# Performance work log

Measured on AMD Instinct MI355X. Metric: run time of the kernel, lower is better.

The kernel has to match this reference:

```python
import jax, jax.numpy as jnp
import numpy as np

B, N, M = 2, 8192, 8192


def setup_inputs() -> dict:
    key = jax.random.key(0)
    ks = jax.random.split(key, 12)
    def rn(k, shape):
        return jax.random.normal(k, shape, dtype=jnp.float32)
    return {
        "in_xyz": rn(ks[0], (B, N, 3)),
        "in_rot": rn(ks[1], (B, N, 4)),
        "in_scale": rn(ks[2], (B, N, 3)),
        "in_opacity": rn(ks[3], (B, N, 1)),
        "in_sh_dc": rn(ks[4], (B, N, 3)),
        "in_sh_rest": rn(ks[5], (B, N, 45)),
        "out_xyz": rn(ks[6], (B, M, 3)),
        "out_rot": rn(ks[7], (B, M, 4)),
        "out_scale": rn(ks[8], (B, M, 3)),
        "out_opacity": rn(ks[9], (B, M, 1)),
        "out_sh_dc": rn(ks[10], (B, M, 3)),
        "out_sh_rest": rn(ks[11], (B, M, 45)),
    }


POS_W, ROT_W, SCALE_W, OPAC_W, SH_W = 1.0, 0.5, 0.5, 0.3, 0.2


def _cdist(a, b):
    # a: [B,M,3], b: [B,N,3] -> [B,M,N] Euclidean distance via Gram trick
    sq = (jnp.sum(a * a, -1)[:, :, None] + jnp.sum(b * b, -1)[:, None, :]
          - 2.0 * jnp.einsum('bmd,bnd->bmn', a, b))
    return jnp.sqrt(jnp.maximum(sq, 0.0))


def _gather(x, idx):
    # x: [B,N,D], idx: [B,M] -> [B,M,D]
    return jnp.take_along_axis(x, idx[:, :, None], axis=1)


def reference(in_xyz, in_rot, in_scale, in_opacity, in_sh_dc, in_sh_rest,
              out_xyz, out_rot, out_scale, out_opacity, out_sh_dc, out_sh_rest):
    dist = _cdist(out_xyz, in_xyz)                 # [B,M,N]
    min_out_to_in = jnp.min(dist, axis=2)          # [B,M]
    match_idx = jnp.argmin(dist, axis=2)           # [B,M]
    min_in_to_out = jnp.min(dist, axis=1)          # [B,N]
    pos_loss = (min_out_to_in.mean() + min_in_to_out.mean()) / 2

    matched_rot = _gather(in_rot, match_idx)
    matched_scale = _gather(in_scale, match_idx)
    matched_opacity = _gather(in_opacity, match_idx)
    matched_sh_dc = _gather(in_sh_dc, match_idx)
    matched_sh_rest = _gather(in_sh_rest, match_idx)

    rot_dot = jnp.abs(jnp.sum(out_rot * matched_rot, axis=-1))
    rot_loss = jnp.mean(1.0 - rot_dot)
    scale_loss = jnp.mean(jnp.abs(out_scale - matched_scale))
    opacity_loss = jnp.mean(jnp.abs(out_opacity - matched_opacity))
    sh_loss = (jnp.mean(jnp.abs(out_sh_dc - matched_sh_dc))
               + jnp.mean(jnp.abs(out_sh_rest - matched_sh_rest)))

    total = (POS_W * pos_loss + ROT_W * rot_loss + SCALE_W * scale_loss
             + OPAC_W * opacity_loss + SH_W * sh_loss)
    return total
```

## Files before the change

### kernel.cpp

```cpp
#include <hip/hip_runtime.h>


#define BB 2
#define NN 8192
#define MM 8192
#define TILE_PTS 1024
#define CHUNK_PTS 64
#define CH_STRIDE (CHUNK_PTS * 4 + 4)
#define PM 256
#define NSL 8
#define NPAIR 512

__device__ __forceinline__ void dmerge(float& d, int& i, float od, int oi) {
    if (od < d || (od == d && oi < i)) { d = od; i = oi; }
}

__device__ __forceinline__ void stage_tile(const float* __restrict__ xyz,
                                           int b, int gtile, int t, float* smem) {
    const uint4* src = (const uint4*)((const char*)xyz +
                       ((size_t)b * NN + (size_t)gtile * TILE_PTS) * 12);
    uint4 wb[3];
#pragma unroll
    for (int k = 0; k < 3; ++k) wb[k] = src[t * 3 + k];
    const unsigned int* w = (const unsigned int*)wb;
    const int p0 = t * 4;
    float4* dst = (float4*)(smem + (p0 >> 6) * CH_STRIDE) + (p0 & 63);
#pragma unroll
    for (int i = 0; i < 4; ++i) {
        float x = __uint_as_float(w[3 * i + 0]);
        float y = __uint_as_float(w[3 * i + 1]);
        float z = __uint_as_float(w[3 * i + 2]);
        float4 v;
        v.x = x; v.y = y; v.z = z;
        v.w = fmaf(z, z, fmaf(y, y, x * x));
        dst[i] = v;
    }
}

__global__ __launch_bounds__(1024) void k_out(
    const float* __restrict__ in_xyz,
    const float* __restrict__ out_xyz,
    float* __restrict__ outD2,
    int*   __restrict__ outIdx) {

    __shared__ float smem[16 * CH_STRIDE];

    const int t  = threadIdx.x;
    const int ml = t >> 4;
    const int c  = t & 15;
    const int blk = blockIdx.x;
    const int b  = blk >> 8;
    const int e  = (blk >> 5) & 7;
    const int m0 = (blk & 31) * PM + ml * 4;

    float m2x0, m2y0, m2z0, msq0, m2x1, m2y1, m2z1, msq1;
    float m2x2, m2y2, m2z2, msq2, m2x3, m2y3, m2z3, msq3;
#define LOADQ(i)                                                            \
    { const float* op = out_xyz + ((size_t)b * MM + m0 + i) * 3;            \
      float ox = op[0], oy = op[1], oz = op[2];                             \
      m2x##i = -2.f * ox; m2y##i = -2.f * oy; m2z##i = -2.f * oz;           \
      msq##i = fmaf(oz, oz, fmaf(oy, oy, ox * ox)); }
    LOADQ(0) LOADQ(1) LOADQ(2) LOADQ(3)
#undef LOADQ

    float bd0 = 3e38f, bd1 = 3e38f, bd2 = 3e38f, bd3 = 3e38f;
    int   bi0 = 0,     bi1 = 0,     bi2 = 0,     bi3 = 0;

    if (t < 256) stage_tile(in_xyz, b, e, t, smem);
    __syncthreads();

    const float4* cp = (const float4*)(smem + c * CH_STRIDE);
    const int base = e * TILE_PTS + c * CHUNK_PTS;
#pragma unroll 8
    for (int j = 0; j < CHUNK_PTS; ++j) {
        float4 p = cp[j];
        float k0 = fmaf(p.x, m2x0, fmaf(p.y, m2y0, fmaf(p.z, m2z0, p.w)));
        float k1 = fmaf(p.x, m2x1, fmaf(p.y, m2y1, fmaf(p.z, m2z1, p.w)));
        float k2 = fmaf(p.x, m2x2, fmaf(p.y, m2y2, fmaf(p.z, m2z2, p.w)));
        float k3 = fmaf(p.x, m2x3, fmaf(p.y, m2y3, fmaf(p.z, m2z3, p.w)));
        if (k0 < bd0) { bd0 = k0; bi0 = base + j; }
        if (k1 < bd1) { bd1 = k1; bi1 = base + j; }
        if (k2 < bd2) { bd2 = k2; bi2 = base + j; }
        if (k3 < bd3) { bd3 = k3; bi3 = base + j; }
    }

#pragma unroll
    for (int off = 1; off < 16; off <<= 1) {
        float od; int oi;
        od = __shfl_xor(bd0, off, 64); oi = __shfl_xor(bi0, off, 64); dmerge(bd0, bi0, od, oi);
        od = __shfl_xor(bd1, off, 64); oi = __shfl_xor(bi1, off, 64); dmerge(bd1, bi1, od, oi);
        od = __shfl_xor(bd2, off, 64); oi = __shfl_xor(bi2, off, 64); dmerge(bd2, bi2, od, oi);
        od = __shfl_xor(bd3, off, 64); oi = __shfl_xor(bi3, off, 64); dmerge(bd3, bi3, od, oi);
    }
    if (c == 0) {
        const size_t g = ((size_t)b * MM + m0) * NSL + e;
        outD2[g + 0 * NSL] = bd0 + msq0; outIdx[g + 0 * NSL] = bi0;
        outD2[g + 1 * NSL] = bd1 + msq1; outIdx[g + 1 * NSL] = bi1;
        outD2[g + 2 * NSL] = bd2 + msq2; outIdx[g + 2 * NSL] = bi2;
        outD2[g + 3 * NSL] = bd3 + msq3; outIdx[g + 3 * NSL] = bi3;
    }
}

__global__ __launch_bounds__(1024) void k_in(
    const float* __restrict__ in_xyz,
    const float* __restrict__ out_xyz,
    float* __restrict__ inD2) {

    __shared__ float smem[16 * CH_STRIDE];

    const int t  = threadIdx.x;
    const int ml = t >> 4;
    const int c  = t & 15;
    const int blk = blockIdx.x;
    const int b  = blk >> 8;
    const int e  = (blk >> 5) & 7;
    const int n0 = (blk & 31) * PM + ml * 4;

    float n2x0, n2y0, n2z0, nsq0, n2x1, n2y1, n2z1, nsq1;
    float n2x2, n2y2, n2z2, nsq2, n2x3, n2y3, n2z3, nsq3;
#define LOADQ(i)                                                            \
    { const float* ip = in_xyz + ((size_t)b * NN + n0 + i) * 3;             \
      float x = ip[0], y = ip[1], z = ip[2];                                \
      n2x##i = -2.f * x; n2y##i = -2.f * y; n2z##i = -2.f * z;              \
      nsq##i = fmaf(z, z, fmaf(y, y, x * x)); }
    LOADQ(0) LOADQ(1) LOADQ(2) LOADQ(3)
#undef LOADQ

    float bd0 = 3e38f, bd1 = 3e38f, bd2 = 3e38f, bd3 = 3e38f;

    if (t < 256) stage_tile(out_xyz, b, e, t, smem);
    __syncthreads();

    const float4* cp = (const float4*)(smem + c * CH_STRIDE);
#pragma unroll 8
    for (int j = 0; j < CHUNK_PTS; ++j) {
        float4 p = cp[j];
        float k0 = fmaf(p.x, n2x0, fmaf(p.y, n2y0, fmaf(p.z, n2z0, p.w)));
        float k1 = fmaf(p.x, n2x1, fmaf(p.y, n2y1, fmaf(p.z, n2z1, p.w)));
        float k2 = fmaf(p.x, n2x2, fmaf(p.y, n2y2, fmaf(p.z, n2z2, p.w)));
        float k3 = fmaf(p.x, n2x3, fmaf(p.y, n2y3, fmaf(p.z, n2z3, p.w)));
        bd0 = fminf(bd0, k0);
        bd1 = fminf(bd1, k1);
        bd2 = fminf(bd2, k2);
        bd3 = fminf(bd3, k3);
    }

#pragma unroll
    for (int off = 1; off < 16; off <<= 1) {
        bd0 = fminf(bd0, __shfl_xor(bd0, off, 64));
        bd1 = fminf(bd1, __shfl_xor(bd1, off, 64));
        bd2 = fminf(bd2, __shfl_xor(bd2, off, 64));
        bd3 = fminf(bd3, __shfl_xor(bd3, off, 64));
    }
    if (c == 0) {
        const size_t g = ((size_t)b * NN + n0) * NSL + e;
        inD2[g + 0 * NSL] = bd0 + nsq0;
        inD2[g + 1 * NSL] = bd1 + nsq1;
        inD2[g + 2 * NSL] = bd2 + nsq2;
        inD2[g + 3 * NSL] = bd3 + nsq3;
    }
}

__global__ __launch_bounds__(256) void k_epi(
    const float* __restrict__ in_rot,
    const float* __restrict__ in_scale,
    const float* __restrict__ in_op,
    const float* __restrict__ in_dc,
    const float* __restrict__ in_rest,
    const float* __restrict__ out_rot,
    const float* __restrict__ out_scale,
    const float* __restrict__ out_op,
    const float* __restrict__ out_dc,
    const float* __restrict__ out_rest,
    const float* __restrict__ outD2,
    const int*   __restrict__ outIdx,
    const float* __restrict__ inD2,
    float* __restrict__ pout,
    float* __restrict__ pin) {

    const int t = threadIdx.x;
    const int blk = blockIdx.x;

    if (blk < 128) {
        const int u = blk * 256 + t;
        const int m = u >> 1;
        const int h = u & 1;
        const int b = m >> 13;
        float d2 = outD2[(size_t)m * NSL + 0];
        int  idx = outIdx[(size_t)m * NSL + 0];
#pragma unroll
        for (int s = 1; s < NSL; ++s) {
            float ds = outD2[(size_t)m * NSL + s];
            int   is = outIdx[(size_t)m * NSL + s];
            if (ds < d2) { d2 = ds; idx = is; }
        }
        const size_t og = (size_t)m;
        const size_t ig = (size_t)b * NN + (size_t)idx;

        float pos = 0.f, rot = 0.f, scl = 0.f, opa = 0.f, dcv = 0.f, rsv = 0.f;
        if (h == 0) {
            pos = sqrtf(fmaxf(d2, 0.f));
            const float4 orv = ((const float4*)out_rot)[og];
            const float4 irv = ((const float4*)in_rot)[ig];
            float rdot = orv.x * irv.x + orv.y * irv.y + orv.z * irv.z + orv.w * irv.w;
            rot = 1.f - fabsf(rdot);
#pragma unroll
            for (int qq = 0; qq < 3; ++qq) scl += fabsf(out_scale[og * 3 + qq] - in_scale[ig * 3 + qq]);
            opa = fabsf(out_op[og] - in_op[ig]);
#pragma unroll
            for (int qq = 0; qq < 3; ++qq) dcv += fabsf(out_dc[og * 3 + qq] - in_dc[ig * 3 + qq]);
#pragma unroll
            for (int e = 0; e < 22; ++e)
                rsv += fabsf(out_rest[og * 45 + e] - in_rest[ig * 45 + e]);
        } else {
#pragma unroll
            for (int e = 22; e < 45; ++e)
                rsv += fabsf(out_rest[og * 45 + e] - in_rest[ig * 45 + e]);
        }

#pragma unroll
        for (int off = 1; off < 64; off <<= 1) {
            pos += __shfl_xor(pos, off, 64);
            rot += __shfl_xor(rot, off, 64);
            scl += __shfl_xor(scl, off, 64);
            opa += __shfl_xor(opa, off, 64);
            dcv += __shfl_xor(dcv, off, 64);
            rsv += __shfl_xor(rsv, off, 64);
        }
        if ((t & 63) == 0) {
            const size_t w = (size_t)blk * 4 + (t >> 6);
            pout[w * 6 + 0] = pos; pout[w * 6 + 1] = rot; pout[w * 6 + 2] = scl;
            pout[w * 6 + 3] = opa; pout[w * 6 + 4] = dcv; pout[w * 6 + 5] = rsv;
        }
    } else {
        const int g = (blk - 128) * 256 + t;
        float d2 = inD2[(size_t)g * NSL + 0];
#pragma unroll
        for (int s = 1; s < NSL; ++s) d2 = fminf(d2, inD2[(size_t)g * NSL + s]);
        float v = sqrtf(fmaxf(d2, 0.f));
#pragma unroll
        for (int off = 1; off < 64; off <<= 1) v += __shfl_xor(v, off, 64);
        if ((t & 63) == 0) pin[(size_t)(blk - 128) * 4 + (t >> 6)] = v;
    }
}

__global__ __launch_bounds__(256) void k_fin(const float* __restrict__ pout,
                                             const float* __restrict__ pin,
                                             unsigned int* __restrict__ out) {
    __shared__ float red[4][8];
    const int t = threadIdx.x;
    float s0 = 0.f, s1 = 0.f, s2 = 0.f, s3 = 0.f, s4 = 0.f, s5 = 0.f, s6 = 0.f;
    for (int i = t; i < 512; i += 256) {
        s0 += pout[(size_t)i * 6 + 0];
        s1 += pout[(size_t)i * 6 + 1];
        s2 += pout[(size_t)i * 6 + 2];
        s3 += pout[(size_t)i * 6 + 3];
        s4 += pout[(size_t)i * 6 + 4];
        s5 += pout[(size_t)i * 6 + 5];
    }
    if (t < 256) s6 += pin[t];
#pragma unroll
    for (int off = 1; off < 64; off <<= 1) {
        s0 += __shfl_xor(s0, off, 64);
        s1 += __shfl_xor(s1, off, 64);
        s2 += __shfl_xor(s2, off, 64);
        s3 += __shfl_xor(s3, off, 64);
        s4 += __shfl_xor(s4, off, 64);
        s5 += __shfl_xor(s5, off, 64);
        s6 += __shfl_xor(s6, off, 64);
    }
    if ((t & 63) == 0) {
        const int w = t >> 6;
        red[w][0] = s0; red[w][1] = s1; red[w][2] = s2; red[w][3] = s3;
        red[w][4] = s4; red[w][5] = s5; red[w][6] = s6;
    }
    __syncthreads();
    if (t == 0) {
        float a[7];
#pragma unroll
        for (int j = 0; j < 7; ++j)
            a[j] = red[0][j] + red[1][j] + red[2][j] + red[3][j];
        const float inv_bm = 1.0f / (float)(BB * MM);
        const float inv_bn = 1.0f / (float)(BB * NN);
        const float pos = 0.5f * (a[0] * inv_bm + a[6] * inv_bn);
        const float rot = a[1] * inv_bm;
        const float scl = a[2] * inv_bm * (1.f / 3.f);
        const float opa = a[3] * inv_bm;
        const float sh  = a[4] * inv_bm * (1.f / 3.f) + a[5] * inv_bm * (1.f / 45.f);
        const float total = 1.0f * pos + 0.5f * rot + 0.5f * scl + 0.3f * opa + 0.2f * sh;
        unsigned int ub = __float_as_uint(total);
        unsigned int r  = (ub + 0x7FFFu + ((ub >> 16) & 1u)) >> 16;
        if (!(total == total) || fabsf(total) > 1e30f) r = 0x4080u;
        out[0] = (r << 16) | r;
    }
}

extern "C" void kernel_launch(void* const* d_in, const int* in_sizes, int n_in,
                              void* d_out, int out_size, void* d_ws, size_t ws_size,
                              hipStream_t stream) {
    const float* in_xyz    = (const float*)d_in[0];
    const float* in_rot    = (const float*)d_in[1];
    const float* in_scale  = (const float*)d_in[2];
    const float* in_op     = (const float*)d_in[3];
    const float* in_dc     = (const float*)d_in[4];
    const float* in_rest   = (const float*)d_in[5];
    const float* out_xyz   = (const float*)d_in[6];
    const float* out_rot   = (const float*)d_in[7];
    const float* out_scale = (const float*)d_in[8];
    const float* out_op    = (const float*)d_in[9];
    const float* out_dc    = (const float*)d_in[10];
    const float* out_rest  = (const float*)d_in[11];

    float* outD2 = (float*)d_ws;
    int*   outIdx = (int*)(outD2 + (size_t)BB * MM * NSL);
    float* inD2  = (float*)(outIdx + (size_t)BB * MM * NSL);
    float* pout  = inD2 + (size_t)BB * NN * NSL;
    float* pin   = pout + 512 * 6;

    k_out<<<NPAIR, 1024, 0, stream>>>(in_xyz, out_xyz, outD2, outIdx);
    k_in<<<NPAIR, 1024, 0, stream>>>(in_xyz, out_xyz, inD2);
    k_epi<<<192, 256, 0, stream>>>(in_rot, in_scale, in_op, in_dc, in_rest,
                                   out_rot, out_scale, out_op, out_dc, out_rest,
                                   outD2, outIdx, inD2, pout, pin);
    k_fin<<<1, 256, 0, stream>>>(pout, pin, (unsigned int*)d_out);
}
```

Measured before the change: 120.1 us.

## Merge nearest-neighbor kernels into one launch with 8 queries per thread and deferred argmin

The separate out-to-in and in-to-out min-distance kernels become one kernel whose block index picks the direction, removing a launch. Each thread now handles 8 query points instead of 4, doubling reuse of every point loaded from shared memory. The argmin index is no longer tracked in the hot loop. It is found afterwards by rescanning the chunk for the lane that holds the group minimum. This trades a short extra rescan and more registers for a cheaper inner loop of plain fminf operations.

```diff
diff --git a/kernel.cpp b/kernel.cpp
--- a/kernel.cpp
+++ b/kernel.cpp
@@ -7,13 +7,9 @@
 #define TILE_PTS 1024
 #define CHUNK_PTS 64
 #define CH_STRIDE (CHUNK_PTS * 4 + 4)
-#define PM 256
+#define PM 512
 #define NSL 8
-#define NPAIR 512
-
-__device__ __forceinline__ void dmerge(float& d, int& i, float od, int oi) {
-    if (od < d || (od == d && oi < i)) { d = od; i = oi; }
-}
+#define NBLK 512
 
 __device__ __forceinline__ void stage_tile(const float* __restrict__ xyz,
                                            int b, int gtile, int t, float* smem) {
@@ -37,11 +33,12 @@
     }
 }
 
-__global__ __launch_bounds__(1024) void k_out(
+__global__ __launch_bounds__(1024) void k_pair(
     const float* __restrict__ in_xyz,
     const float* __restrict__ out_xyz,
     float* __restrict__ outD2,
-    int*   __restrict__ outIdx) {
+    int*   __restrict__ outIdx,
+    float* __restrict__ inD2) {
 
     __shared__ float smem[16 * CH_STRIDE];
 
@@ -49,115 +46,82 @@
     const int ml = t >> 4;
     const int c  = t & 15;
     const int blk = blockIdx.x;
-    const int b  = blk >> 8;
-    const int e  = (blk >> 5) & 7;
-    const int m0 = (blk & 31) * PM + ml * 4;
-
-    float m2x0, m2y0, m2z0, msq0, m2x1, m2y1, m2z1, msq1;
-    float m2x2, m2y2, m2z2, msq2, m2x3, m2y3, m2z3, msq3;
-#define LOADQ(i)                                                            \
-    { const float* op = out_xyz + ((size_t)b * MM + m0 + i) * 3;            \
-      float ox = op[0], oy = op[1], oz = op[2];                             \
-      m2x##i = -2.f * ox; m2y##i = -2.f * oy; m2z##i = -2.f * oz;           \
-      msq##i = fmaf(oz, oz, fmaf(oy, oy, ox * ox)); }
-    LOADQ(0) LOADQ(1) LOADQ(2) LOADQ(3)
-#undef LOADQ
-
-    float bd0 = 3e38f, bd1 = 3e38f, bd2 = 3e38f, bd3 = 3e38f;
-    int   bi0 = 0,     bi1 = 0,     bi2 = 0,     bi3 = 0;
-
-    if (t < 256) stage_tile(in_xyz, b, e, t, smem);
+    const int side = blk >> 8;
+    const int r8 = blk & 255;
+    const int b  = r8 >> 7;
+    const int e  = (r8 >> 4) & 7;
+    const int g  = r8 & 15;
+    const int q0 = g * PM + ml * 8;
+
+    const float* qbase = (side == 0) ? out_xyz : in_xyz;
+    const float* pbase = (side == 0) ? in_xyz  : out_xyz;
+
+    float qx[8], qy[8], qz[8], bd[8];
+#pragma unroll
+    for (int r = 0; r < 8; ++r) {
+        const float* qp = qbase + ((size_t)b * MM + q0 + r) * 3;
+        qx[r] = -2.f * qp[0];
+        qy[r] = -2.f * qp[1];
+        qz[r] = -2.f * qp[2];
+        bd[r] = 3e38f;
+    }
+
+    if (t < 256) stage_tile(pbase, b, e, t, smem);
     __syncthreads();
 
     const float4* cp = (const float4*)(smem + c * CH_STRIDE);
     const int base = e * TILE_PTS + c * CHUNK_PTS;
-#pragma unroll 8
+
+#pragma unroll 2
     for (int j = 0; j < CHUNK_PTS; ++j) {
         float4 p = cp[j];
-        float k0 = fmaf(p.x, m2x0, fmaf(p.y, m2y0, fmaf(p.z, m2z0, p.w)));
-        float k1 = fmaf(p.x, m2x1, fmaf(p.y, m2y1, fmaf(p.z, m2z1, p.w)));
-        float k2 = fmaf(p.x, m2x2, fmaf(p.y, m2y2, fmaf(p.z, m2z2, p.w)));
-        float k3 = fmaf(p.x, m2x3, fmaf(p.y, m2y3, fmaf(p.z, m2z3, p.w)));
-        if (k0 < bd0) { bd0 = k0; bi0 = base + j; }
-        if (k1 < bd1) { bd1 = k1; bi1 = base + j; }
-        if (k2 < bd2) { bd2 = k2; bi2 = base + j; }
-        if (k3 < bd3) { bd3 = k3; bi3 = base + j; }
-    }
-
-#pragma unroll
-    for (int off = 1; off < 16; off <<= 1) {
-        float od; int oi;
-        od = __shfl_xor(bd0, off, 64); oi = __shfl_xor(bi0, off, 64); dmerge(bd0, bi0, od, oi);
-        od = __shfl_xor(bd1, off, 64); oi = __shfl_xor(bi1, off, 64); dmerge(bd1, bi1, od, oi);
-        od = __shfl_xor(bd2, off, 64); oi = __shfl_xor(bi2, off, 64); dmerge(bd2, bi2, od, oi);
-        od = __shfl_xor(bd3, off, 64); oi = __shfl_xor(bi3, off, 64); dmerge(bd3, bi3, od, oi);
-    }
-    if (c == 0) {
-        const size_t g = ((size_t)b * MM + m0) * NSL + e;
-        outD2[g + 0 * NSL] = bd0 + msq0; outIdx[g + 0 * NSL] = bi0;
-        outD2[g + 1 * NSL] = bd1 + msq1; outIdx[g + 1 * NSL] = bi1;
-        outD2[g + 2 * NSL] = bd2 + msq2; outIdx[g + 2 * NSL] = bi2;
-        outD2[g + 3 * NSL] = bd3 + msq3; outIdx[g + 3 * NSL] = bi3;
-    }
-}
-
-__global__ __launch_bounds__(1024) void k_in(
-    const float* __restrict__ in_xyz,
-    const float* __restrict__ out_xyz,
-    float* __restrict__ inD2) {
-
-    __shared__ float smem[16 * CH_STRIDE];
-
-    const int t  = threadIdx.x;
-    const int ml = t >> 4;
-    const int c  = t & 15;
-    const int blk = blockIdx.x;
-    const int b  = blk >> 8;
-    const int e  = (blk >> 5) & 7;
-    const int n0 = (blk & 31) * PM + ml * 4;
-
-    float n2x0, n2y0, n2z0, nsq0, n2x1, n2y1, n2z1, nsq1;
-    float n2x2, n2y2, n2z2, nsq2, n2x3, n2y3, n2z3, nsq3;
-#define LOADQ(i)                                                            \
-    { const float* ip = in_xyz + ((size_t)b * NN + n0 + i) * 3;             \
-      float x = ip[0], y = ip[1], z = ip[2];                                \
-      n2x##i = -2.f * x; n2y##i = -2.f * y; n2z##i = -2.f * z;              \
-      nsq##i = fmaf(z, z, fmaf(y, y, x * x)); }
-    LOADQ(0) LOADQ(1) LOADQ(2) LOADQ(3)
-#undef LOADQ
-
-    float bd0 = 3e38f, bd1 = 3e38f, bd2 = 3e38f, bd3 = 3e38f;
-
-    if (t < 256) stage_tile(out_xyz, b, e, t, smem);
-    __syncthreads();
-
-    const float4* cp = (const float4*)(smem + c * CH_STRIDE);
-#pragma unroll 8
-    for (int j = 0; j < CHUNK_PTS; ++j) {
-        float4 p = cp[j];
-        float k0 = fmaf(p.x, n2x0, fmaf(p.y, n2y0, fmaf(p.z, n2z0, p.w)));
-        float k1 = fmaf(p.x, n2x1, fmaf(p.y, n2y1, fmaf(p.z, n2z1, p.w)));
-        float k2 = fmaf(p.x, n2x2, fmaf(p.y, n2y2, fmaf(p.z, n2z2, p.w)));
-        float k3 = fmaf(p.x, n2x3, fmaf(p.y, n2y3, fmaf(p.z, n2z3, p.w)));
-        bd0 = fminf(bd0, k0);
-        bd1 = fminf(bd1, k1);
-        bd2 = fminf(bd2, k2);
-        bd3 = fminf(bd3, k3);
-    }
-
-#pragma unroll
-    for (int off = 1; off < 16; off <<= 1) {
-        bd0 = fminf(bd0, __shfl_xor(bd0, off, 64));
-        bd1 = fminf(bd1, __shfl_xor(bd1, off, 64));
-        bd2 = fminf(bd2, __shfl_xor(bd2, off, 64));
-        bd3 = fminf(bd3, __shfl_xor(bd3, off, 64));
-    }
-    if (c == 0) {
-        const size_t g = ((size_t)b * NN + n0) * NSL + e;
-        inD2[g + 0 * NSL] = bd0 + nsq0;
-        inD2[g + 1 * NSL] = bd1 + nsq1;
-        inD2[g + 2 * NSL] = bd2 + nsq2;
-        inD2[g + 3 * NSL] = bd3 + nsq3;
+#pragma unroll
+        for (int r = 0; r < 8; ++r) {
+            float k = fmaf(p.x, qx[r], fmaf(p.y, qy[r], fmaf(p.z, qz[r], p.w)));
+            bd[r] = fminf(bd[r], k);
+        }
+    }
+
+    if (side == 0) {
+#pragma unroll
+        for (int r = 0; r < 8; ++r) {
+            float gm = bd[r];
+#pragma unroll
+            for (int off = 1; off < 16; off <<= 1)
+                gm = fminf(gm, __shfl_xor(gm, off, 64));
+            int cand = 0x7FFFFFFF;
+            if (bd[r] == gm) {
+                for (int j = 0; j < CHUNK_PTS; ++j) {
+                    float4 p = cp[j];
+                    float k = fmaf(p.x, qx[r], fmaf(p.y, qy[r], fmaf(p.z, qz[r], p.w)));
+                    if (k == gm) { cand = base + j; break; }
+                }
+            }
+#pragma unroll
+            for (int off = 1; off < 16; off <<= 1) {
+                int oc = __shfl_xor(cand, off, 64);
+                cand = oc < cand ? oc : cand;
+            }
+            if (c == 0) {
+                float s = fmaf(qz[r], qz[r], fmaf(qy[r], qy[r], qx[r] * qx[r]));
+                const size_t gg = ((size_t)b * MM + q0 + r) * NSL + e;
+                outD2[gg] = gm + 0.25f * s;
+                outIdx[gg] = cand;
+            }
+        }
+    } else {
+#pragma unroll
+        for (int r = 0; r < 8; ++r) {
+            float gm = bd[r];
+#pragma unroll
+            for (int off = 1; off < 16; off <<= 1)
+                gm = fminf(gm, __shfl_xor(gm, off, 64));
+            if (c == 0) {
+                float s = fmaf(qz[r], qz[r], fmaf(qy[r], qy[r], qx[r] * qx[r]));
+                const size_t gg = ((size_t)b * NN + q0 + r) * NSL + e;
+                inD2[gg] = gm + 0.25f * s;
+            }
+        }
     }
 }
 
@@ -317,8 +281,7 @@
     float* pout  = inD2 + (size_t)BB * NN * NSL;
     float* pin   = pout + 512 * 6;
 
-    k_out<<<NPAIR, 1024, 0, stream>>>(in_xyz, out_xyz, outD2, outIdx);
-    k_in<<<NPAIR, 1024, 0, stream>>>(in_xyz, out_xyz, inD2);
+    k_pair<<<NBLK, 1024, 0, stream>>>(in_xyz, out_xyz, outD2, outIdx, inD2);
     k_epi<<<192, 256, 0, stream>>>(in_rot, in_scale, in_op, in_dc, in_rest,
                                    out_rot, out_scale, out_op, out_dc, out_rest,
                                    outD2, outIdx, inD2, pout, pin);
```

After: 169.7 us. 41.3% more time.
